# Performance work log

Measured on AMD Instinct MI355X. Metric: run time of the kernel, lower is better.

The kernel has to match this reference:

```python
import jax, jax.numpy as jnp
import numpy as np

N_NODES = 100000
N_EDGES = 3200000
D_IN = 256
D_OUT = 256


def setup_inputs() -> dict:
    key = jax.random.key(0)
    k1, k2, k3, k4, k5 = jax.random.split(key, 5)
    inputs = jax.random.normal(k1, (N_NODES, D_IN), dtype=jnp.float32)
    adj_row = jax.random.randint(k2, (N_EDGES,), 0, N_NODES, dtype=jnp.int32)
    adj_col = jax.random.randint(k3, (N_EDGES,), 0, N_NODES, dtype=jnp.int32)
    adj_val = jax.random.uniform(k4, (N_EDGES,), dtype=jnp.float32)
    # xavier-uniform init for weight, zeros for bias (as in reset_parameters)
    limit = float(np.sqrt(6.0 / (D_IN + D_OUT)))
    weight = jax.random.uniform(k5, (D_IN, D_OUT), dtype=jnp.float32,
                                minval=-limit, maxval=limit)
    bias = jnp.zeros((D_OUT,), dtype=jnp.float32)
    return {"inputs": inputs, "adj_row": adj_row, "adj_col": adj_col,
            "adj_val": adj_val, "weight": weight, "bias": bias}


def reference(inputs, adj_row, adj_col, adj_val, weight, bias) -> jnp.ndarray:
    # support = X @ W  -> [N, D_OUT]
    support = inputs @ weight
    # SpMM: out[r] = sum_{e: row[e]==r} val[e] * support[col[e]]
    gathered = support[adj_col] * adj_val[:, None]          # [E, D_OUT]
    output = jax.ops.segment_sum(gathered, adj_row, num_segments=N_NODES)
    return output + bias
```

## Files before the change

kernel.cpp:

```cpp
#include <hip/hip_runtime.h>

#define N_NODES 100000
#define N_EDGES 3200000
#define D 256
#define NBLK ((N_NODES + 255) / 256)
#define GEMM_TILES (N_NODES / 32)
#define GEMM_BLOCKS ((GEMM_TILES + 3) / 4)
#define HIST_BLOCKS (N_EDGES / 256)
#define ZERO_BLOCKS NBLK
#define WSH_BLOCKS 32

#define RPB 16
#define NB_BUCKETS (N_NODES / RPB)
#define P2_CAP 4096

using u16 = unsigned short;
using u32 = unsigned int;

typedef __attribute__((ext_vector_type(8))) short bf16x8;
typedef __attribute__((ext_vector_type(4))) float f32x4;

__device__ inline u16 f2bf(float f) {
    u32 x = __builtin_bit_cast(u32, f);
    return (u16)((x + 0x7FFFu + ((x >> 16) & 1u)) >> 16);
}
__device__ inline float bf2f(u16 u) {
    return __builtin_bit_cast(float, (u32)u << 16);
}

__global__ __launch_bounds__(256) void prep_kernel(
    const float* __restrict__ W, u16* __restrict__ Wf, int* __restrict__ cnt)
{
    if (blockIdx.x < ZERO_BLOCKS) {
        const int i = blockIdx.x * 256 + threadIdx.x;
        if (i < N_NODES) cnt[i] = 0;
        return;
    }
    const int t = (blockIdx.x - ZERO_BLOCKS) * 256 + threadIdx.x;
    const int kt = t >> 10;
    const int nt = (t >> 6) & 15;
    const int lane = t & 63;
    const int kbase = kt * 32 + ((lane >> 4) * 8);
    const int n = nt * 16 + (lane & 15);
    u16 frag[8];
    #pragma unroll
    for (int j = 0; j < 8; ++j)
        frag[j] = f2bf(W[(size_t)(kbase + j) * D + n]);
    #pragma unroll
    for (int j = 0; j < 8; ++j)
        Wf[(size_t)t * 8 + j] = frag[j];
}

__global__ __launch_bounds__(256) void gemm_hist_kernel(
    const float* __restrict__ X, const u16* __restrict__ Wf,
    u16* __restrict__ S, const int* __restrict__ row, int* __restrict__ cnt)
{
    if (blockIdx.x >= GEMM_BLOCKS) {
        const int e = (blockIdx.x - GEMM_BLOCKS) * 256 + threadIdx.x;
        atomicAdd(&cnt[row[e]], 1);
        return;
    }
    const int lane = threadIdx.x & 63;
    const int tile = blockIdx.x * 4 + (threadIdx.x >> 6);
    if (tile >= GEMM_TILES) return;
    const int row0 = tile * 32;
    const int m = lane & 15;
    const int quad = lane >> 4;

    f32x4 acc0[16], acc1[16];
    #pragma unroll
    for (int t = 0; t < 16; ++t) {
        acc0[t] = (f32x4){0.f, 0.f, 0.f, 0.f};
        acc1[t] = (f32x4){0.f, 0.f, 0.f, 0.f};
    }

    const float* xA = X + (size_t)(row0 + m) * D + quad * 8;
    const float* xB = X + (size_t)(row0 + 16 + m) * D + quad * 8;
    const bf16x8* __restrict__ Bf = (const bf16x8*)Wf;

    for (int k0 = 0; k0 < 8; ++k0) {
        const float4 a0l = *(const float4*)(xA + k0 * 32);
        const float4 a0h = *(const float4*)(xA + k0 * 32 + 4);
        const float4 a1l = *(const float4*)(xB + k0 * 32);
        const float4 a1h = *(const float4*)(xB + k0 * 32 + 4);
        bf16x8 a0, a1;
        a0[0] = (short)f2bf(a0l.x); a0[1] = (short)f2bf(a0l.y);
        a0[2] = (short)f2bf(a0l.z); a0[3] = (short)f2bf(a0l.w);
        a0[4] = (short)f2bf(a0h.x); a0[5] = (short)f2bf(a0h.y);
        a0[6] = (short)f2bf(a0h.z); a0[7] = (short)f2bf(a0h.w);
        a1[0] = (short)f2bf(a1l.x); a1[1] = (short)f2bf(a1l.y);
        a1[2] = (short)f2bf(a1l.z); a1[3] = (short)f2bf(a1l.w);
        a1[4] = (short)f2bf(a1h.x); a1[5] = (short)f2bf(a1h.y);
        a1[6] = (short)f2bf(a1h.z); a1[7] = (short)f2bf(a1h.w);

        const bf16x8* bp = Bf + (size_t)k0 * 1024 + lane;
        #pragma unroll
        for (int g = 0; g < 4; ++g) {
            const bf16x8 b0 = bp[g * 256 + 0];
            const bf16x8 b1 = bp[g * 256 + 64];
            const bf16x8 b2 = bp[g * 256 + 128];
            const bf16x8 b3 = bp[g * 256 + 192];
            acc0[g*4+0] = __builtin_amdgcn_mfma_f32_16x16x32_bf16(a0, b0, acc0[g*4+0], 0, 0, 0);
            acc1[g*4+0] = __builtin_amdgcn_mfma_f32_16x16x32_bf16(a1, b0, acc1[g*4+0], 0, 0, 0);
            acc0[g*4+1] = __builtin_amdgcn_mfma_f32_16x16x32_bf16(a0, b1, acc0[g*4+1], 0, 0, 0);
            acc1[g*4+1] = __builtin_amdgcn_mfma_f32_16x16x32_bf16(a1, b1, acc1[g*4+1], 0, 0, 0);
            acc0[g*4+2] = __builtin_amdgcn_mfma_f32_16x16x32_bf16(a0, b2, acc0[g*4+2], 0, 0, 0);
            acc1[g*4+2] = __builtin_amdgcn_mfma_f32_16x16x32_bf16(a1, b2, acc1[g*4+2], 0, 0, 0);
            acc0[g*4+3] = __builtin_amdgcn_mfma_f32_16x16x32_bf16(a0, b3, acc0[g*4+3], 0, 0, 0);
            acc1[g*4+3] = __builtin_amdgcn_mfma_f32_16x16x32_bf16(a1, b3, acc1[g*4+3], 0, 0, 0);
        }
    }

    #pragma unroll
    for (int nt = 0; nt < 16; ++nt) {
        u16* Sp = S + (size_t)(nt >> 3) * ((size_t)N_NODES * 128);
        const int cip = (nt & 7) * 16 + m;
        #pragma unroll
        for (int i = 0; i < 4; ++i) {
            Sp[(size_t)(row0 + quad * 4 + i) * 128 + cip]      = f2bf(acc0[nt][i]);
            Sp[(size_t)(row0 + 16 + quad * 4 + i) * 128 + cip] = f2bf(acc1[nt][i]);
        }
    }
}

__global__ __launch_bounds__(256) void blocksum_kernel(
    const int* __restrict__ cnt, int* __restrict__ bsum)
{
    __shared__ int sh[4];
    const int i = blockIdx.x * 256 + threadIdx.x;
    int x = (i < N_NODES) ? cnt[i] : 0;
    #pragma unroll
    for (int off = 32; off > 0; off >>= 1) x += __shfl_xor(x, off);
    if ((threadIdx.x & 63) == 0) sh[threadIdx.x >> 6] = x;
    __syncthreads();
    if (threadIdx.x == 0) bsum[blockIdx.x] = sh[0] + sh[1] + sh[2] + sh[3];
}

__global__ __launch_bounds__(512) void bscan_kernel(
    const int* __restrict__ bsum, int* __restrict__ boff, int* __restrict__ starts)
{
    __shared__ int wsum[8];
    const int tid = threadIdx.x, lane = tid & 63, wv = tid >> 6;
    const int c = (tid < NBLK) ? bsum[tid] : 0;
    int x = c;
    #pragma unroll
    for (int off = 1; off < 64; off <<= 1) {
        int y = __shfl_up(x, off);
        if (lane >= off) x += y;
    }
    if (lane == 63) wsum[wv] = x;
    __syncthreads();
    if (tid == 0) {
        int run = 0;
        #pragma unroll
        for (int w = 0; w < 8; ++w) { int t = wsum[w]; wsum[w] = run; run += t; }
        starts[N_NODES] = N_EDGES;
    }
    __syncthreads();
    if (tid < NBLK) boff[tid] = x - c + wsum[wv];
}

__global__ __launch_bounds__(256) void localscan_kernel(
    const int* __restrict__ cnt, const int* __restrict__ boff,
    int* __restrict__ starts, int* __restrict__ bcur)
{
    __shared__ int wsum[4];
    const int tid = threadIdx.x, lane = tid & 63, wv = tid >> 6;
    const int i = blockIdx.x * 256 + tid;
    const int c = (i < N_NODES) ? cnt[i] : 0;
    int x = c;
    #pragma unroll
    for (int off = 1; off < 64; off <<= 1) {
        int y = __shfl_up(x, off);
        if (lane >= off) x += y;
    }
    if (lane == 63) wsum[wv] = x;
    __syncthreads();
    if (tid == 0) {
        int run = 0;
        #pragma unroll
        for (int w = 0; w < 4; ++w) { int t = wsum[w]; wsum[w] = run; run += t; }
    }
    __syncthreads();
    const int excl = x - c + wsum[wv] + boff[blockIdx.x];
    if (i < N_NODES) {
        starts[i] = excl;
        if ((i & (RPB - 1)) == 0) bcur[i / RPB] = excl;
    }
}

__global__ __launch_bounds__(256) void binplace_kernel(
    const int* __restrict__ row, const int* __restrict__ col,
    const float* __restrict__ val, int* __restrict__ bcur,
    uint2* __restrict__ pce)
{
    const int e = blockIdx.x * 256 + threadIdx.x;
    const int r = row[e];
    const u32 c = (u32)col[e];
    const float v = val[e];
    const int pos = atomicAdd(&bcur[r / RPB], 1);
    pce[pos] = make_uint2(c | ((u32)(r & (RPB - 1)) << 17),
                          __builtin_bit_cast(u32, v));
}

__global__ __launch_bounds__(256) void bucketsort_kernel(
    const int* __restrict__ starts, uint2* __restrict__ pce)
{
    __shared__ uint2 ent[P2_CAP];
    __shared__ int rbase[RPB + 1];
    __shared__ int rcnt[RPB];
    const int b = blockIdx.x;
    const int tid = threadIdx.x;
    if (tid <= RPB) rbase[tid] = starts[b * RPB + tid];
    if (tid < RPB) rcnt[tid] = 0;
    __syncthreads();
    const int base = rbase[0];
    const int n = rbase[RPB] - base;
    for (int i = tid; i < n; i += 256) ent[i] = pce[base + i];
    __syncthreads();
    for (int i = tid; i < n; i += 256) {
        const uint2 e = ent[i];
        const int rlow = (int)((e.x >> 17) & (u32)(RPB - 1));
        const int rank = atomicAdd(&rcnt[rlow], 1);
        pce[rbase[rlow] + rank] = make_uint2(e.x & 0x1FFFFu, e.y);
    }
}

__global__ __launch_bounds__(256) void reduce_kernel(
    const u16* __restrict__ S, const int* __restrict__ starts,
    const uint2* __restrict__ pce, const float* __restrict__ bias,
    float* __restrict__ out, int plane)
{
    const int lane = threadIdx.x & 63;
    const int r = blockIdx.x * 4 + (threadIdx.x >> 6);
    const int s0 = starts[r];
    const int s1 = starts[r + 1];

    const u32* __restrict__ Sp =
        (const u32*)(S + (size_t)plane * ((size_t)N_NODES * 128));
    float2 acc = make_float2(0.f, 0.f);

    for (int base = s0; base < s1; base += 64) {
        const int n = min(64, s1 - base);
        uint2 pr = make_uint2(0u, 0u);
        if (lane < n) pr = pce[base + lane];
        const int c = (int)pr.x;
        const float v = __builtin_bit_cast(float, pr.y);

        int i = 0;
        for (; i + 8 <= n; i += 8) {
            int cc[8]; float vv[8]; u32 s[8];
            #pragma unroll
            for (int u = 0; u < 8; ++u) {
                cc[u] = __shfl(c, i + u);
                vv[u] = __shfl(v, i + u);
            }
            #pragma unroll
            for (int u = 0; u < 8; ++u)
                s[u] = Sp[(size_t)cc[u] * 64 + lane];
            #pragma unroll
            for (int u = 0; u < 8; ++u) {
                acc.x += vv[u] * bf2f((u16)(s[u] & 0xFFFFu));
                acc.y += vv[u] * bf2f((u16)(s[u] >> 16));
            }
        }
        for (; i < n; ++i) {
            const int c0 = __shfl(c, i);
            const float v0 = __shfl(v, i);
            const u32 a0 = Sp[(size_t)c0 * 64 + lane];
            acc.x += v0 * bf2f((u16)(a0 & 0xFFFFu));
            acc.y += v0 * bf2f((u16)(a0 >> 16));
        }
    }

    const float2 b2 = ((const float2*)bias)[plane * 64 + lane];
    acc.x += b2.x; acc.y += b2.y;
    ((float2*)out)[(size_t)r * 128 + plane * 64 + lane] = acc;
}

extern "C" void kernel_launch(void* const* d_in, const int* in_sizes, int n_in,
                              void* d_out, int out_size, void* d_ws, size_t ws_size,
                              hipStream_t stream) {
    const float* X    = (const float*)d_in[0];
    const int*   row  = (const int*)d_in[1];
    const int*   col  = (const int*)d_in[2];
    const float* val  = (const float*)d_in[3];
    const float* W    = (const float*)d_in[4];
    const float* bias = (const float*)d_in[5];
    float* out = (float*)d_out;

    char* ws = (char*)d_ws;
    u16*   Sx     = (u16*)ws;
    int*   starts = (int*)(ws + 51200000);
    uint2* pce    = (uint2*)(ws + 51600064);
    int*   cnt    = (int*)(ws + 51600064);
    u16*   Wf     = (u16*)(ws + 77200064);
    int*   bsum   = (int*)(ws + 77331136);
    int*   boff   = (int*)(ws + 77333184);
    int*   bcur   = (int*)(ws + 77335232);

    prep_kernel<<<ZERO_BLOCKS + WSH_BLOCKS, 256, 0, stream>>>(W, Wf, cnt);

    gemm_hist_kernel<<<GEMM_BLOCKS + HIST_BLOCKS, 256, 0, stream>>>(X, Wf, Sx, row, cnt);

    blocksum_kernel<<<NBLK, 256, 0, stream>>>(cnt, bsum);
    bscan_kernel<<<1, 512, 0, stream>>>(bsum, boff, starts);
    localscan_kernel<<<NBLK, 256, 0, stream>>>(cnt, boff, starts, bcur);

    binplace_kernel<<<N_EDGES / 256, 256, 0, stream>>>(row, col, val, bcur, pce);
    bucketsort_kernel<<<NB_BUCKETS, 256, 0, stream>>>(starts, pce);

    reduce_kernel<<<N_NODES / 4, 256, 0, stream>>>(Sx, starts, pce, bias, out, 0);
    reduce_kernel<<<N_NODES / 4, 256, 0, stream>>>(Sx, starts, pce, bias, out, 1);
}
```

Before: 717.7 us.

## Replace global per-row atomic histogram with shared-memory per-bucket histograms

The per-row global atomic histogram that was fused into the GEMM launch is replaced by a separate kernel. It builds per-bucket (16-row) counts in LDS for each of 256 edge slices, then a column-sum kernel reduces them and the scan runs over 6250 buckets instead of 100000 rows. Per-row start offsets are now computed inside bucketsort by counting row-low bits in shared memory. This removes contended global atomics and shrinks the scan, at the cost of a 6.4MB partial-histogram write and read, and the histogram no longer overlaps with the GEMM.

```diff
diff --git a/kernel.cpp b/kernel.cpp
--- a/kernel.cpp
+++ b/kernel.cpp
@@ -3,16 +3,17 @@
 #define N_NODES 100000
 #define N_EDGES 3200000
 #define D 256
-#define NBLK ((N_NODES + 255) / 256)
 #define GEMM_TILES (N_NODES / 32)
 #define GEMM_BLOCKS ((GEMM_TILES + 3) / 4)
-#define HIST_BLOCKS (N_EDGES / 256)
-#define ZERO_BLOCKS NBLK
 #define WSH_BLOCKS 32
 
 #define RPB 16
 #define NB_BUCKETS (N_NODES / RPB)
+#define NBLK_B ((NB_BUCKETS + 255) / 256)
 #define P2_CAP 4096
+
+#define HIST_P 256
+#define EDGES_PER_HB (N_EDGES / HIST_P)
 
 using u16 = unsigned short;
 using u32 = unsigned int;
@@ -29,14 +30,9 @@
 }
 
 __global__ __launch_bounds__(256) void prep_kernel(
-    const float* __restrict__ W, u16* __restrict__ Wf, int* __restrict__ cnt)
-{
-    if (blockIdx.x < ZERO_BLOCKS) {
-        const int i = blockIdx.x * 256 + threadIdx.x;
-        if (i < N_NODES) cnt[i] = 0;
-        return;
-    }
-    const int t = (blockIdx.x - ZERO_BLOCKS) * 256 + threadIdx.x;
+    const float* __restrict__ W, u16* __restrict__ Wf)
+{
+    const int t = blockIdx.x * 256 + threadIdx.x;
     const int kt = t >> 10;
     const int nt = (t >> 6) & 15;
     const int lane = t & 63;
@@ -51,15 +47,10 @@
         Wf[(size_t)t * 8 + j] = frag[j];
 }
 
-__global__ __launch_bounds__(256) void gemm_hist_kernel(
+__global__ __launch_bounds__(256) void gemm_kernel(
     const float* __restrict__ X, const u16* __restrict__ Wf,
-    u16* __restrict__ S, const int* __restrict__ row, int* __restrict__ cnt)
-{
-    if (blockIdx.x >= GEMM_BLOCKS) {
-        const int e = (blockIdx.x - GEMM_BLOCKS) * 256 + threadIdx.x;
-        atomicAdd(&cnt[row[e]], 1);
-        return;
-    }
+    u16* __restrict__ S)
+{
     const int lane = threadIdx.x & 63;
     const int tile = blockIdx.x * 4 + (threadIdx.x >> 6);
     if (tile >= GEMM_TILES) return;
@@ -123,12 +114,34 @@
     }
 }
 
-__global__ __launch_bounds__(256) void blocksum_kernel(
-    const int* __restrict__ cnt, int* __restrict__ bsum)
+__global__ __launch_bounds__(1024) void hist_kernel(
+    const int* __restrict__ row, u32* __restrict__ hglob)
+{
+    __shared__ u32 h[NB_BUCKETS];
+    const int tid = threadIdx.x;
+    for (int j = tid; j < NB_BUCKETS; j += 1024) h[j] = 0u;
+    __syncthreads();
+    const int e0 = blockIdx.x * EDGES_PER_HB;
+    for (int i = tid; i < EDGES_PER_HB; i += 1024)
+        atomicAdd(&h[row[e0 + i] >> 4], 1u);
+    __syncthreads();
+    u32* dst = hglob + (size_t)blockIdx.x * NB_BUCKETS;
+    for (int j = tid; j < NB_BUCKETS; j += 1024) dst[j] = h[j];
+}
+
+__global__ __launch_bounds__(256) void colsum_kernel(
+    const u32* __restrict__ hglob, u32* __restrict__ tot, int* __restrict__ bsum)
 {
     __shared__ int sh[4];
-    const int i = blockIdx.x * 256 + threadIdx.x;
-    int x = (i < N_NODES) ? cnt[i] : 0;
+    const int b = blockIdx.x * 256 + threadIdx.x;
+    u32 s = 0u;
+    if (b < NB_BUCKETS) {
+        #pragma unroll 8
+        for (int p = 0; p < HIST_P; ++p)
+            s += hglob[(size_t)p * NB_BUCKETS + b];
+        tot[b] = s;
+    }
+    int x = (int)s;
     #pragma unroll
     for (int off = 32; off > 0; off >>= 1) x += __shfl_xor(x, off);
     if ((threadIdx.x & 63) == 0) sh[threadIdx.x >> 6] = x;
@@ -136,38 +149,33 @@
     if (threadIdx.x == 0) bsum[blockIdx.x] = sh[0] + sh[1] + sh[2] + sh[3];
 }
 
-__global__ __launch_bounds__(512) void bscan_kernel(
-    const int* __restrict__ bsum, int* __restrict__ boff, int* __restrict__ starts)
-{
-    __shared__ int wsum[8];
-    const int tid = threadIdx.x, lane = tid & 63, wv = tid >> 6;
-    const int c = (tid < NBLK) ? bsum[tid] : 0;
+__global__ __launch_bounds__(64) void bscan_kernel(
+    const int* __restrict__ bsum, int* __restrict__ boff,
+    int* __restrict__ starts, int* __restrict__ bstart)
+{
+    const int tid = threadIdx.x;
+    const int c = (tid < NBLK_B) ? bsum[tid] : 0;
     int x = c;
     #pragma unroll
     for (int off = 1; off < 64; off <<= 1) {
         int y = __shfl_up(x, off);
-        if (lane >= off) x += y;
-    }
-    if (lane == 63) wsum[wv] = x;
-    __syncthreads();
+        if (tid >= off) x += y;
+    }
+    if (tid < NBLK_B) boff[tid] = x - c;
     if (tid == 0) {
-        int run = 0;
-        #pragma unroll
-        for (int w = 0; w < 8; ++w) { int t = wsum[w]; wsum[w] = run; run += t; }
         starts[N_NODES] = N_EDGES;
-    }
-    __syncthreads();
-    if (tid < NBLK) boff[tid] = x - c + wsum[wv];
-}
-
-__global__ __launch_bounds__(256) void localscan_kernel(
-    const int* __restrict__ cnt, const int* __restrict__ boff,
-    int* __restrict__ starts, int* __restrict__ bcur)
+        bstart[NB_BUCKETS] = N_EDGES;
+    }
+}
+
+__global__ __launch_bounds__(256) void blocalscan_kernel(
+    const u32* __restrict__ tot, const int* __restrict__ boff,
+    int* __restrict__ bstart, int* __restrict__ bcur)
 {
     __shared__ int wsum[4];
     const int tid = threadIdx.x, lane = tid & 63, wv = tid >> 6;
     const int i = blockIdx.x * 256 + tid;
-    const int c = (i < N_NODES) ? cnt[i] : 0;
+    const int c = (i < NB_BUCKETS) ? (int)tot[i] : 0;
     int x = c;
     #pragma unroll
     for (int off = 1; off < 64; off <<= 1) {
@@ -183,10 +191,7 @@
     }
     __syncthreads();
     const int excl = x - c + wsum[wv] + boff[blockIdx.x];
-    if (i < N_NODES) {
-        starts[i] = excl;
-        if ((i & (RPB - 1)) == 0) bcur[i / RPB] = excl;
-    }
+    if (i < NB_BUCKETS) { bstart[i] = excl; bcur[i] = excl; }
 }
 
 __global__ __launch_bounds__(256) void binplace_kernel(
@@ -204,25 +209,36 @@
 }
 
 __global__ __launch_bounds__(256) void bucketsort_kernel(
-    const int* __restrict__ starts, uint2* __restrict__ pce)
+    const int* __restrict__ bstart, uint2* __restrict__ pce,
+    int* __restrict__ starts)
 {
     __shared__ uint2 ent[P2_CAP];
-    __shared__ int rbase[RPB + 1];
     __shared__ int rcnt[RPB];
+    __shared__ int rcur[RPB];
     const int b = blockIdx.x;
     const int tid = threadIdx.x;
-    if (tid <= RPB) rbase[tid] = starts[b * RPB + tid];
+    const int base = bstart[b];
+    const int n = bstart[b + 1] - base;
     if (tid < RPB) rcnt[tid] = 0;
     __syncthreads();
-    const int base = rbase[0];
-    const int n = rbase[RPB] - base;
     for (int i = tid; i < n; i += 256) ent[i] = pce[base + i];
+    __syncthreads();
+    for (int i = tid; i < n; i += 256)
+        atomicAdd(&rcnt[(ent[i].x >> 17) & (RPB - 1)], 1);
+    __syncthreads();
+    if (tid == 0) {
+        int run = 0;
+        #pragma unroll
+        for (int j = 0; j < RPB; ++j) { rcur[j] = run; run += rcnt[j]; }
+    }
+    __syncthreads();
+    if (tid < RPB) starts[b * RPB + tid] = base + rcur[tid];
     __syncthreads();
     for (int i = tid; i < n; i += 256) {
         const uint2 e = ent[i];
-        const int rlow = (int)((e.x >> 17) & (u32)(RPB - 1));
-        const int rank = atomicAdd(&rcnt[rlow], 1);
-        pce[rbase[rlow] + rank] = make_uint2(e.x & 0x1FFFFu, e.y);
+        const int rl = (int)((e.x >> 17) & (u32)(RPB - 1));
+        const int pos = atomicAdd(&rcur[rl], 1);
+        pce[base + pos] = make_uint2(e.x & 0x1FFFFu, e.y);
     }
 }
 
@@ -293,22 +309,25 @@
     u16*   Sx     = (u16*)ws;
     int*   starts = (int*)(ws + 51200000);
     uint2* pce    = (uint2*)(ws + 51600064);
-    int*   cnt    = (int*)(ws + 51600064);
     u16*   Wf     = (u16*)(ws + 77200064);
-    int*   bsum   = (int*)(ws + 77331136);
-    int*   boff   = (int*)(ws + 77333184);
-    int*   bcur   = (int*)(ws + 77335232);
-
-    prep_kernel<<<ZERO_BLOCKS + WSH_BLOCKS, 256, 0, stream>>>(W, Wf, cnt);
-
-    gemm_hist_kernel<<<GEMM_BLOCKS + HIST_BLOCKS, 256, 0, stream>>>(X, Wf, Sx, row, cnt);
-
-    blocksum_kernel<<<NBLK, 256, 0, stream>>>(cnt, bsum);
-    bscan_kernel<<<1, 512, 0, stream>>>(bsum, boff, starts);
-    localscan_kernel<<<NBLK, 256, 0, stream>>>(cnt, boff, starts, bcur);
+    u32*   hglob  = (u32*)(ws + 77331136);
+    u32*   tot    = (u32*)(ws + 83731136);
+    int*   bsum   = (int*)(ws + 83756736);
+    int*   boff   = (int*)(ws + 83757760);
+    int*   bstart = (int*)(ws + 83758784);
+    int*   bcur   = (int*)(ws + 83784384);
+
+    prep_kernel<<<WSH_BLOCKS, 256, 0, stream>>>(W, Wf);
+
+    gemm_kernel<<<GEMM_BLOCKS, 256, 0, stream>>>(X, Wf, Sx);
+
+    hist_kernel<<<HIST_P, 1024, 0, stream>>>(row, hglob);
+    colsum_kernel<<<NBLK_B, 256, 0, stream>>>(hglob, tot, bsum);
+    bscan_kernel<<<1, 64, 0, stream>>>(bsum, boff, starts, bstart);
+    blocalscan_kernel<<<NBLK_B, 256, 0, stream>>>(tot, boff, bstart, bcur);
 
     binplace_kernel<<<N_EDGES / 256, 256, 0, stream>>>(row, col, val, bcur, pce);
-    bucketsort_kernel<<<NB_BUCKETS, 256, 0, stream>>>(starts, pce);
+    bucketsort_kernel<<<NB_BUCKETS, 256, 0, stream>>>(bstart, pce, starts);
 
     reduce_kernel<<<N_NODES / 4, 256, 0, stream>>>(Sx, starts, pce, bias, out, 0);
     reduce_kernel<<<N_NODES / 4, 256, 0, stream>>>(Sx, starts, pce, bias, out, 1);
```

Result: faster. 623.9 us (-13.1%).
